# Optimization experiments

Measured on AMD Instinct MI355X. Metric: run time of the kernel, lower is better.

Reference implementation:

```python
import jax, jax.numpy as jnp
import numpy as np

EPS = 1e-5

def layernorm(x, w, b):
    mu = x.mean(-1, keepdims=True)
    var = x.var(-1, keepdims=True)
    return (x - mu) / jnp.sqrt(var + EPS) * w + b

def silu(x):
    return x * jax.nn.sigmoid(x)

def causal_dwconv(x, w, b):
    # x: (B,L,D), w: (D,K) depthwise causal conv along L
    K = w.shape[1]
    xt = jnp.moveaxis(x, 1, 2)                      # (B,D,L)
    xt = jnp.pad(xt, ((0, 0), (0, 0), (K - 1, 0)))
    y = jax.lax.conv_general_dilated(xt, w[:, None, :], (1,), 'VALID',
        dimension_numbers=('NCH', 'OIH', 'NCH'), feature_group_count=w.shape[0])
    return jnp.moveaxis(y + b[None, :, None], 2, 1)

def mamba_layer(x, p):
    # LayerNorm + Mamba selective scan; returns (out, C) with C the per-step C projection ("C_fast")
    xn = layernorm(x, p['ln_w'], p['ln_b'])
    xz = xn @ p['in_proj_w']                        # (B,L,2*Di)
    Di = p['conv_w'].shape[0]
    xh, z = xz[..., :Di], xz[..., Di:]
    xh = silu(causal_dwconv(xh, p['conv_w'], p['conv_b']))
    dbl = xh @ p['x_proj_w']                        # (B,L,R+2*S)
    R = p['dt_proj_w'].shape[0]
    S = p['A_log'].shape[1]
    dt = jax.nn.softplus(dbl[..., :R] @ p['dt_proj_w'] + p['dt_proj_b'])  # (B,L,Di)
    Bm = dbl[..., R:R + S]                          # (B,L,S)
    Cm = dbl[..., R + S:]                           # (B,L,S)
    A = -jnp.exp(p['A_log'])                        # (Di,S)
    dA = jnp.exp(dt[..., None] * A)                 # (B,L,Di,S)
    dBx = dt[..., None] * Bm[:, :, None, :] * xh[..., None]
    def step(h, inp):
        a, bx = inp
        h = a * h + bx
        return h, h
    h0 = jnp.zeros((x.shape[0], Di, S), x.dtype)
    _, hs = jax.lax.scan(step, h0, (jnp.moveaxis(dA, 1, 0), jnp.moveaxis(dBx, 1, 0)))
    y = jnp.einsum('lbds,bls->bld', hs, Cm) + p['D'] * xh
    y = y * silu(z)
    return y @ p['out_proj_w'], Cm

def run_chunks(x, k, p):
    # contiguous L-chunks folded into batch (chunks are independent sequences)
    B, L, D = x.shape
    y, C = mamba_layer(x.reshape(B * k, L // k, D), p)
    return y.reshape(B, L, D), C.reshape(B, k, L // k, -1)

def batchnorm(h, g, b):
    mu = h.mean((0, 1))
    var = h.var((0, 1))
    return (h - mu) / jnp.sqrt(var + EPS) * g + b

def freq_ffn(x, fc1_w, bn1_g, bn1_b, r_mat, i_mat, rb, ib, fc2_w, bn2_g, bn2_b):
    h = jax.nn.relu(batchnorm(jnp.einsum('bnc,hc->bnh', x, fc1_w), bn1_g, bn1_b))
    xf = jnp.fft.fft(h, axis=1, norm='ortho')
    # torch einsum 'bnc,cc->bnc' multiplies by the DIAGONAL of the matrix
    rd = jnp.diagonal(r_mat)
    idg = jnp.diagonal(i_mat)
    xr = jax.nn.relu(xf.real * rd - xf.imag * idg + rb)
    xi = jax.nn.relu(xf.imag * rd + xf.real * idg + ib)
    h = jnp.fft.ifft(xr + 1j * xi, axis=1, norm='ortho').real.astype(x.dtype)
    return batchnorm(jnp.einsum('bnh,ch->bnc', h, fc2_w), bn2_g, bn2_b)


def setup_inputs() -> dict:
    key = jax.random.key(0)
    B, L, D = 4, 512, 128
    Di, S, R, K, H = 256, 64, 8, 4, 256
    ks = jax.random.split(key, 16)
    rn = lambda k, sh, s=1.0: (jax.random.normal(k, sh) * s).astype(jnp.float32)
    return {
        'x': rn(ks[0], (B, L, D)),
        'ln_w': jnp.ones((D,), jnp.float32), 'ln_b': jnp.zeros((D,), jnp.float32),
        'in_proj_w': rn(ks[1], (D, 2 * Di), D ** -0.5),
        'conv_w': rn(ks[2], (Di, K), 0.3),
        'conv_b': jnp.zeros((Di,), jnp.float32),
        'x_proj_w': rn(ks[3], (Di, R + 2 * S), Di ** -0.5),
        'dt_proj_w': rn(ks[4], (R, Di), R ** -0.5),
        'dt_proj_b': rn(ks[5], (Di,), 0.1) - 4.0,
        'A_log': jnp.log(jnp.tile(jnp.arange(1, S + 1, dtype=jnp.float32), (Di, 1))),
        'D_param': jnp.ones((Di,), jnp.float32),
        'out_proj_w': rn(ks[6], (Di, D), Di ** -0.5),
        'norm1_w': jnp.ones((D,), jnp.float32), 'norm1_b': jnp.zeros((D,), jnp.float32),
        'norm2_w': jnp.ones((D,), jnp.float32), 'norm2_b': jnp.zeros((D,), jnp.float32),
        'fc1_w': rn(ks[7], (H, D), D ** -0.5),
        'bn1_g': jnp.ones((H,), jnp.float32), 'bn1_b': jnp.zeros((H,), jnp.float32),
        'r_mat': rn(ks[8], (H, H), 0.02),
        'i_mat': rn(ks[9], (H, H), 0.02),
        'rb': rn(ks[10], (H,), 0.02),
        'ib': rn(ks[11], (H,), 0.02),
        'fc2_w': rn(ks[12], (D, H), H ** -0.5),
        'bn2_g': jnp.ones((D,), jnp.float32), 'bn2_b': jnp.zeros((D,), jnp.float32),
    }


def reference(x, ln_w, ln_b, in_proj_w, conv_w, conv_b, x_proj_w, dt_proj_w, dt_proj_b,
              A_log, D_param, out_proj_w, norm1_w, norm1_b, norm2_w, norm2_b,
              fc1_w, bn1_g, bn1_b, r_mat, i_mat, rb, ib, fc2_w, bn2_g, bn2_b):
    p = dict(ln_w=ln_w, ln_b=ln_b, in_proj_w=in_proj_w, conv_w=conv_w, conv_b=conv_b,
             x_proj_w=x_proj_w, dt_proj_w=dt_proj_w, dt_proj_b=dt_proj_b,
             A_log=A_log, D=D_param, out_proj_w=out_proj_w)
    x_o, C0 = mamba_layer(x, p)                 # full sequence
    y1, C1 = run_chunks(x, 2, p)                # 2 halves
    y2, C2 = run_chunks(x, 4, p)                # 4 quarters
    y3, C3 = run_chunks(x, 8, p)                # 8 eighths
    x_o = x_o + y1 + y2 + y3                    # drop_path = Identity
    xo = x + layernorm(x_o, norm1_w, norm1_b)
    out = xo + freq_ffn(layernorm(xo, norm2_w, norm2_b),
                        fc1_w, bn1_g, bn1_b, r_mat, i_mat, rb, ib, fc2_w, bn2_g, bn2_b)
    return out, C0, C1, C2, C3
```

## Files before the change

kernel.cpp:

```cpp
#include <hip/hip_runtime.h>
#include <hip/hip_bf16.h>
#include <math.h>


constexpr int NT = 2048;
constexpr int Di = 256;
constexpr float EPSF = 1e-5f;
constexpr float LOG2E = 1.4426950408889634f;
constexpr float ISQ512 = 0.04419417382415922f;

typedef __attribute__((ext_vector_type(8))) short short8;
typedef __attribute__((ext_vector_type(4))) float f32x4;

constexpr long O_CS2B  = 0;
constexpr long O_CSIB  = 262144;
constexpr long O_A2    = 524288;
constexpr long O_FC1B  = 540672;
constexpr long O_FC2B  = 557056;
constexpr long O_INPB  = 573440;
constexpr long O_XPB2  = 606208;
constexpr long O_OPB   = 663552;
constexpr long O_RD    = 679936;
constexpr long O_IDG   = 680192;
constexpr long O_XNB   = 680448;
constexpr long O_XZB   = 811520;
constexpr long O_XHB   = 1335808;
constexpr long O_DBLX  = 2384384;
constexpr long O_DTDX  = 5595648;
constexpr long O_BCT   = 7692800;
constexpr long O_YS    = 8741376;
constexpr long O_XO    = 10838528;
constexpr long O_LN2B  = 11100672;
constexpr long O_H1B   = 11231744;
constexpr long O_H1NTB = 11493888;
constexpr long O_XRITB = 11756032;
constexpr long O_H2B   = 12280320;
constexpr long O_F2B   = 12542464;
constexpr long O_SQ1   = 12673536;
constexpr long O_SQ2   = 12674048;
constexpr long O_XO1   = O_XRITB;
constexpr long O_YACCB = O_DBLX;

__device__ __forceinline__ ushort bf16bits(float v) {
  __hip_bfloat16 h = __float2bfloat16(v);
  return *(ushort*)&h;
}
__device__ __forceinline__ float bfu(ushort u) {
  return __uint_as_float((uint)u << 16);
}

__global__ __launch_bounds__(256) void k_tables(
    const float* __restrict__ A_log, const float* __restrict__ fc1_w,
    const float* __restrict__ fc2_w, const float* __restrict__ r_mat,
    const float* __restrict__ i_mat, const float* __restrict__ in_proj_w,
    const float* __restrict__ x_proj_w, const float* __restrict__ dt_proj_w,
    const float* __restrict__ out_proj_w,
    const float* __restrict__ x, const float* __restrict__ ln_w,
    const float* __restrict__ ln_b, float* __restrict__ ws) {
  __shared__ float ct[512];
  int tid = threadIdx.x;
  ct[tid]       = __cosf((float)tid * (6.283185307179586f / 512.0f)) * ISQ512;
  ct[tid + 256] = __cosf((float)(tid + 256) * (6.283185307179586f / 512.0f)) * ISQ512;
  __syncthreads();
  __hip_bfloat16* cs2b = (__hip_bfloat16*)(ws + O_CS2B);
  __hip_bfloat16* csib = (__hip_bfloat16*)(ws + O_CSIB);
  int i = blockIdx.x * 256 + tid;
  if (i < 524288) {
    int r = i >> 9, n = i & 511;
    float v;
    if (r < 512) v = ct[(r * n) & 511];
    else         v = -ct[((r - 512) * n + 384) & 511];
    cs2b[i] = __float2bfloat16(v);
  } else {
    int j = i - 524288;
    int n = j >> 10, kp = j & 1023;
    float v;
    if (kp < 512) v = ct[(n * kp) & 511];
    else          v = -ct[(n * (kp - 512) + 384) & 511];
    csib[j] = __float2bfloat16(v);
  }
  if (i < 16384) ws[O_A2 + i] = -expf(A_log[i]) * LOG2E;
  if (i < 32768) {
    ((__hip_bfloat16*)(ws + O_FC1B))[i] = __float2bfloat16(fc1_w[i]);
    ((__hip_bfloat16*)(ws + O_FC2B))[i] = __float2bfloat16(fc2_w[i]);
  }
  if (i < 65536) {
    int n = i >> 7, k = i & 127;
    ((__hip_bfloat16*)(ws + O_INPB))[i] = __float2bfloat16(in_proj_w[k * 512 + n]);
  }
  if (i < 114688) {
    int n = i >> 8, k = i & 255;
    float v = 0.f;
    if (n < 136) v = x_proj_w[k * 136 + n];
    else if (n < 392) {
      int d = n - 136;
#pragma unroll
      for (int r = 0; r < 8; ++r) v = fmaf(x_proj_w[k * 136 + r], dt_proj_w[r * 256 + d], v);
    }
    ((__hip_bfloat16*)(ws + O_XPB2))[i] = __float2bfloat16(v);
  }
  if (i >= 131072 && i < 163840) {
    int j = i - 131072;
    int n = j >> 8, k = j & 255;
    ((__hip_bfloat16*)(ws + O_OPB))[j] = __float2bfloat16(out_proj_w[k * 128 + n]);
  }
  if (i < 256) {
    ws[O_RD + i] = r_mat[i * 256 + i];
    ws[O_IDG + i] = i_mat[i * 256 + i];
  }
  if (i < 512) ws[O_SQ1 + i] = 0.f;
  if (i < 256) ws[O_SQ2 + i] = 0.f;
  if (blockIdx.x < 512) {
    ushort* outb = (ushort*)(ws + O_XNB);
    int lane = tid & 63;
    int t = (blockIdx.x * 256 + tid) >> 6;
    float v0 = x[t * 128 + lane], v1 = x[t * 128 + 64 + lane];
    float s = v0 + v1, sq = v0 * v0 + v1 * v1;
#pragma unroll
    for (int off = 32; off; off >>= 1) { s += __shfl_xor(s, off); sq += __shfl_xor(sq, off); }
    float mu = s * (1.f / 128.f);
    float rstd = rsqrtf(sq * (1.f / 128.f) - mu * mu + EPSF);
    outb[t * 128 + lane]      = bf16bits((v0 - mu) * rstd * ln_w[lane] + ln_b[lane]);
    outb[t * 128 + 64 + lane] = bf16bits((v1 - mu) * rstd * ln_w[64 + lane] + ln_b[64 + lane]);
  }
}

__global__ void k_lndbl(const float* __restrict__ x, const float* __restrict__ xo1,
                        const float* __restrict__ w1, const float* __restrict__ b1,
                        const float* __restrict__ w2, const float* __restrict__ b2,
                        float* __restrict__ xo, ushort* __restrict__ ln2b) {
  int lane = threadIdx.x & 63;
  int t = (blockIdx.x * 256 + threadIdx.x) >> 6;
  float u0 = xo1[t * 128 + lane], u1 = xo1[t * 128 + 64 + lane];
  float s = u0 + u1, sq = u0 * u0 + u1 * u1;
#pragma unroll
  for (int off = 32; off; off >>= 1) { s += __shfl_xor(s, off); sq += __shfl_xor(sq, off); }
  float mu = s * (1.f / 128.f);
  float rstd = rsqrtf(sq * (1.f / 128.f) - mu * mu + EPSF);
  float a0 = x[t * 128 + lane]      + (u0 - mu) * rstd * w1[lane] + b1[lane];
  float a1 = x[t * 128 + 64 + lane] + (u1 - mu) * rstd * w1[64 + lane] + b1[64 + lane];
  xo[t * 128 + lane] = a0;
  xo[t * 128 + 64 + lane] = a1;
  s = a0 + a1; sq = a0 * a0 + a1 * a1;
#pragma unroll
  for (int off = 32; off; off >>= 1) { s += __shfl_xor(s, off); sq += __shfl_xor(sq, off); }
  mu = s * (1.f / 128.f);
  rstd = rsqrtf(sq * (1.f / 128.f) - mu * mu + EPSF);
  ln2b[t * 128 + lane]      = bf16bits((a0 - mu) * rstd * w2[lane] + b2[lane]);
  ln2b[t * 128 + 64 + lane] = bf16bits((a1 - mu) * rstd * w2[64 + lane] + b2[64 + lane]);
}

template <bool OUTBF16>
__global__ __launch_bounds__(256) void k_gmfma(const ushort* __restrict__ A,
                                               const ushort* __restrict__ Bt,
                                               void* __restrict__ Cv,
                                               int M, int N, int K,
                                               long sA, long sBt, long sC) {
  A += (long)blockIdx.z * sA;
  Bt += (long)blockIdx.z * sBt;
  int lane = threadIdx.x & 63, wid = threadIdx.x >> 6;
  int m0 = blockIdx.y * 64 + wid * 16, n0 = blockIdx.x * 64;
  const ushort* arow = A + (long)(m0 + (lane & 15)) * K + (lane >> 4) * 8;
  const ushort* brow = Bt + (long)(n0 + (lane & 15)) * K + (lane >> 4) * 8;
  f32x4 acc0 = {0.f, 0.f, 0.f, 0.f}, acc1 = acc0, acc2 = acc0, acc3 = acc0;
#pragma unroll 4
  for (int k0 = 0; k0 < K; k0 += 32) {
    short8 av = *(const short8*)(arow + k0);
    short8 b0 = *(const short8*)(brow + k0);
    short8 b1 = *(const short8*)(brow + 16L * K + k0);
    short8 b2 = *(const short8*)(brow + 32L * K + k0);
    short8 b3 = *(const short8*)(brow + 48L * K + k0);
    acc0 = __builtin_amdgcn_mfma_f32_16x16x32_bf16(av, b0, acc0, 0, 0, 0);
    acc1 = __builtin_amdgcn_mfma_f32_16x16x32_bf16(av, b1, acc1, 0, 0, 0);
    acc2 = __builtin_amdgcn_mfma_f32_16x16x32_bf16(av, b2, acc2, 0, 0, 0);
    acc3 = __builtin_amdgcn_mfma_f32_16x16x32_bf16(av, b3, acc3, 0, 0, 0);
  }
  int r0 = (lane >> 4) * 4, c0 = lane & 15;
#pragma unroll
  for (int j = 0; j < 4; ++j) {
    long row = m0 + r0 + j;
    float v[4] = {acc0[j], acc1[j], acc2[j], acc3[j]};
    if (OUTBF16) {
      __hip_bfloat16* C = (__hip_bfloat16*)Cv + blockIdx.z * sC;
#pragma unroll
      for (int c = 0; c < 4; ++c) {
        int n = n0 + c * 16 + c0;
        if (n < N) C[row * N + n] = __float2bfloat16(v[c]);
      }
    } else {
      float* C = (float*)Cv + blockIdx.z * sC;
#pragma unroll
      for (int c = 0; c < 4; ++c) {
        int n = n0 + c * 16 + c0;
        if (n < N) C[row * N + n] = v[c];
      }
    }
  }
}

__global__ __launch_bounds__(256) void k_gmfma_bn(const ushort* __restrict__ A,
                                                  const ushort* __restrict__ Bt,
                                                  ushort* __restrict__ C,
                                                  float* __restrict__ SQ,
                                                  int N, int K) {
  int lane = threadIdx.x & 63, wid = threadIdx.x >> 6;
  int m0 = blockIdx.y * 64 + wid * 16, n0 = blockIdx.x * 64;
  const ushort* arow = A + (long)(m0 + (lane & 15)) * K + (lane >> 4) * 8;
  const ushort* brow = Bt + (long)(n0 + (lane & 15)) * K + (lane >> 4) * 8;
  f32x4 acc[4] = {{0.f, 0.f, 0.f, 0.f}, {0.f, 0.f, 0.f, 0.f},
                  {0.f, 0.f, 0.f, 0.f}, {0.f, 0.f, 0.f, 0.f}};
#pragma unroll 4
  for (int k0 = 0; k0 < K; k0 += 32) {
    short8 av = *(const short8*)(arow + k0);
#pragma unroll
    for (int c = 0; c < 4; ++c) {
      short8 bv = *(const short8*)(brow + (long)c * 16 * K + k0);
      acc[c] = __builtin_amdgcn_mfma_f32_16x16x32_bf16(av, bv, acc[c], 0, 0, 0);
    }
  }
  int r0 = (lane >> 4) * 4, c0 = lane & 15;
#pragma unroll
  for (int j = 0; j < 4; ++j) {
    long row = m0 + r0 + j;
#pragma unroll
    for (int c = 0; c < 4; ++c)
      C[row * N + n0 + c * 16 + c0] = bf16bits(acc[c][j]);
  }
#pragma unroll
  for (int c = 0; c < 4; ++c) {
    f32x4 v = acc[c];
    float s = v[0] + v[1] + v[2] + v[3];
    float q = v[0] * v[0] + v[1] * v[1] + v[2] * v[2] + v[3] * v[3];
    s += __shfl_xor(s, 16); s += __shfl_xor(s, 32);
    q += __shfl_xor(q, 16); q += __shfl_xor(q, 32);
    if ((lane >> 4) == 0) {
      int n = n0 + c * 16 + c0;
      atomicAdd(&SQ[n], s);
      atomicAdd(&SQ[N + n], q);
    }
  }
}

__global__ void k_conv4(const ushort* __restrict__ xzb, const float* __restrict__ cw,
                        const float* __restrict__ cb, ushort* __restrict__ xhb) {
  int i = blockIdx.x * 256 + threadIdx.x;
  int t = i >> 8, d = i & 255;
  float w0 = cw[d * 4 + 0], w1 = cw[d * 4 + 1], w2 = cw[d * 4 + 2], w3 = cw[d * 4 + 3];
  float bias = cb[d];
  float x0  = bfu(xzb[(long)t * 512 + d]);
  float xm1 = t >= 1 ? bfu(xzb[(long)(t - 1) * 512 + d]) : 0.f;
  float xm2 = t >= 2 ? bfu(xzb[(long)(t - 2) * 512 + d]) : 0.f;
  float xm3 = t >= 3 ? bfu(xzb[(long)(t - 3) * 512 + d]) : 0.f;
  if ((t & 63) >= 3) {
    float s = fmaf(w0, xm3, fmaf(w1, xm2, fmaf(w2, xm1, fmaf(w3, x0, bias))));
    float sil = s / (1.f + expf(-s));
    ushort sb = bf16bits(sil);
#pragma unroll
    for (int v = 0; v < 4; ++v) xhb[v * 524288 + i] = sb;
  } else {
#pragma unroll
    for (int v = 0; v < 4; ++v) {
      int lv = t & ((512 >> v) - 1);
      float s = fmaf(w3, x0, bias);
      if (lv >= 1) s = fmaf(w2, xm1, s);
      if (lv >= 2) s = fmaf(w1, xm2, s);
      if (lv >= 3) s = fmaf(w0, xm3, s);
      float sil = s / (1.f + expf(-s));
      xhb[v * 524288 + i] = bf16bits(sil);
    }
  }
}

__global__ __launch_bounds__(256) void k_prep(const float* __restrict__ dblx,
                                              const ushort* __restrict__ xhb,
                                              const float* __restrict__ dt_b,
                                              float* __restrict__ outC,
                                              uint* __restrict__ DTDX,
                                              float* __restrict__ BCT) {
  int t0 = blockIdx.x * 64, task = blockIdx.y, v = blockIdx.z;
  int tid = threadIdx.x;
  const float* dp = dblx + ((long)v * 2048 + t0) * 392;
  if (task < 4) {
    __shared__ uint tile[64][65];
    int d0 = task * 64;
#pragma unroll
    for (int it = 0; it < 16; ++it) {
      int idx = it * 256 + tid;
      int t = idx >> 6, dl = idx & 63;
      int d = d0 + dl;
      float logit = dp[(long)t * 392 + 136 + d] + dt_b[d];
      float dtv = fmaxf(logit, 0.f) + log1pf(expf(-fabsf(logit)));
      float xv = bfu(xhb[((long)v * 2048 + t0 + t) * 256 + d]);
      tile[t][dl] = ((uint)bf16bits(dtv * xv) << 16) | (uint)bf16bits(dtv);
    }
    __syncthreads();
#pragma unroll
    for (int it = 0; it < 16; ++it) {
      int idx = it * 256 + tid;
      int dl = idx >> 6, t = idx & 63;
      DTDX[((long)(v * 256 + d0 + dl)) * 2048 + t0 + t] = tile[t][dl];
    }
  } else if (task < 6) {
    int j0 = (task - 4) * 64;
    float* bout = BCT + ((long)v * 2048 + t0) * 128;
#pragma unroll
    for (int it = 0; it < 16; ++it) {
      int idx = it * 256 + tid;
      int t = idx >> 6, j = (idx & 63) + j0;
      bout[(long)t * 128 + j] = dp[(long)t * 392 + 8 + j];
    }
  } else {
#pragma unroll
    for (int it = 0; it < 16; ++it) {
      int idx = it * 256 + tid;
      int t = idx >> 6, s = idx & 63;
      outC[(long)v * 131072 + (long)(t0 + t) * 64 + s] = dp[(long)t * 392 + 72 + s];
    }
  }
}

template <int CTRL>
__device__ __forceinline__ float dpp_add(float x) {
  int t = __builtin_amdgcn_update_dpp(0, __float_as_int(x), CTRL, 0xF, 0xF, true);
  return x + __int_as_float(t);
}

__global__ __launch_bounds__(256) void k_scan(const uint* __restrict__ DTDX,
                                              const float* __restrict__ BCT,
                                              const float* __restrict__ A2,
                                              float* __restrict__ ys) {
  int lane = threadIdx.x & 63;
  int gwid = (blockIdx.x * 256 + threadIdx.x) >> 6;
  int v, base;
  if (gwid < 1024)      { v = 0; base = 0; }
  else if (gwid < 3072) { v = 1; base = 1024; }
  else if (gwid < 7168) { v = 2; base = 3072; }
  else                  { v = 3; base = 7168; }
  int local = gwid - base;
  int b = local >> 8, d = local & 255;
  int Lp = 512 >> v;
  int t0 = b * Lp;
  const uint* drow = DTDX + ((long)(v * 256 + d)) * 2048 + t0;
  const float* brow = BCT + ((long)(v * 2048 + t0)) * 128;
  float* ysp = ys + (long)v * NT * Di + (long)((b << 8) + d) * Lp;
  float a2 = A2[d * 64 + lane];
  float h = 0.f;

#define LOADG(BB, CC, G)                                                     \
  { const float* rg = rowp + (G) * 1024;                                     \
    _Pragma("unroll") for (int q = 0; q < 8; ++q) {                          \
      BB[q] = rg[q * 128 + lane];                                            \
      CC[q] = rg[q * 128 + 64 + lane];                                       \
    } }
#define PROCG(BB, CC, G)                                                     \
  _Pragma("unroll") for (int q = 0; q < 8; ++q) {                            \
    const int l2 = (G) * 8 + q;                                              \
    uint u = (uint)__builtin_amdgcn_readlane((int)rdx, l2);                  \
    float sdt = __uint_as_float(u << 16);                                    \
    float sdx = __uint_as_float(u & 0xffff0000u);                            \
    float a = __builtin_amdgcn_exp2f(sdt * a2);                              \
    h = fmaf(a, h, sdx * BB[q]);                                             \
    float p = h * CC[q];                                                     \
    p = dpp_add<0x111>(p); p = dpp_add<0x112>(p);                            \
    p = dpp_add<0x114>(p); p = dpp_add<0x118>(p);                            \
    p = dpp_add<0x142>(p); p = dpp_add<0x143>(p);                            \
    int tot = __builtin_amdgcn_readlane(__float_as_int(p), 63);              \
    asm("v_writelane_b32 %0, %1, %2" : "+v"(ybuf_i) : "s"(tot), "i"(l2));    \
  }

  for (int c = 0; c < Lp; c += 64) {
    uint rdx = drow[c + lane];
    const float* rowp = brow + (long)c * 128;
    int ybuf_i = 0;
    float b0[8], c0[8], b1[8], c1[8];
    LOADG(b0, c0, 0)
    LOADG(b1, c1, 1)
    PROCG(b0, c0, 0) LOADG(b0, c0, 2)
    PROCG(b1, c1, 1) LOADG(b1, c1, 3)
    PROCG(b0, c0, 2) LOADG(b0, c0, 4)
    PROCG(b1, c1, 3) LOADG(b1, c1, 5)
    PROCG(b0, c0, 4) LOADG(b0, c0, 6)
    PROCG(b1, c1, 5) LOADG(b1, c1, 7)
    PROCG(b0, c0, 6)
    PROCG(b1, c1, 7)
    ysp[c + lane] = __int_as_float(ybuf_i);
  }
#undef LOADG
#undef PROCG
}

__global__ void k_yfull(const float* __restrict__ ys, const ushort* __restrict__ xhb,
                        const ushort* __restrict__ xzb, const float* __restrict__ Dp,
                        ushort* __restrict__ yaccb) {
  int i = blockIdx.x * 256 + threadIdx.x;
  int t = i >> 8, d = i & 255;
  float z = bfu(xzb[(long)t * 512 + 256 + d]);
  float sil = z / (1.f + expf(-z));
  float Dd = Dp[d];
  float s = 0.f;
#pragma unroll
  for (int v = 0; v < 4; ++v) {
    int Lp = 512 >> v;
    int b = t >> (9 - v);
    int l = t & (Lp - 1);
    float ysv = ys[(long)v * NT * Di + (long)((b << 8) + d) * Lp + l];
    float xhv = bfu(xhb[(long)v * 524288 + i]);
    s += ysv + Dd * xhv;
  }
  yaccb[i] = bf16bits(s * sil);
}

__global__ __launch_bounds__(256) void k_bnreluT(const ushort* __restrict__ h1b,
                                                 const float* __restrict__ SQ,
                                                 const float* __restrict__ g,
                                                 const float* __restrict__ bb,
                                                 ushort* __restrict__ outT) {
  __shared__ float tile[64][65];
  __shared__ float sc_s[64], sh_s[64];
  int t0 = blockIdx.x * 64, f0 = blockIdx.y * 64, b = blockIdx.z;
  int tid = threadIdx.x;
  if (tid < 64) {
    int f = f0 + tid;
    float mu = SQ[f] * (1.f / NT);
    float var = SQ[256 + f] * (1.f / NT) - mu * mu;
    float sc = g[f] * rsqrtf(var + EPSF);
    sc_s[tid] = sc;
    sh_s[tid] = bb[f] - mu * sc;
  }
  __syncthreads();
  const uint* h1u = (const uint*)h1b;
#pragma unroll
  for (int i = 0; i < 8; ++i) {
    int idx = i * 256 + tid;
    int r = idx >> 5, cu = idx & 31;
    uint u = h1u[((long)(b * 512 + t0 + r)) * 128 + (f0 >> 1) + cu];
    int c = cu * 2;
    tile[r][c]     = fmaxf(fmaf(bfu((ushort)(u & 0xffff)), sc_s[c], sh_s[c]), 0.f);
    tile[r][c + 1] = fmaxf(fmaf(bfu((ushort)(u >> 16)), sc_s[c + 1], sh_s[c + 1]), 0.f);
  }
  __syncthreads();
  int tc2 = (tid & 31) * 2, fr0 = tid >> 5;
#pragma unroll
  for (int i = 0; i < 8; ++i) {
    int fr = fr0 + i * 8;
    uint u = ((uint)bf16bits(tile[tc2 + 1][fr]) << 16) | bf16bits(tile[tc2][fr]);
    long off = (long)b * 131072 + (long)(f0 + fr) * 512 + t0 + tc2;
    *(uint*)(outT + off) = u;
  }
}

__global__ __launch_bounds__(256) void k_dftfreq(const ushort* __restrict__ CS2B,
                                                 const ushort* __restrict__ H1NTB,
                                                 const float* __restrict__ rd,
                                                 const float* __restrict__ idg,
                                                 const float* __restrict__ rb,
                                                 const float* __restrict__ ib,
                                                 ushort* __restrict__ XRITB) {
  int b = blockIdx.z;
  int lane = threadIdx.x & 63, wid = threadIdx.x >> 6;
  int m0 = blockIdx.y * 64 + wid * 16;
  int n0 = blockIdx.x * 64;
  const ushort* acrow = CS2B + (long)(m0 + (lane & 15)) * 512 + (lane >> 4) * 8;
  const ushort* asrow = acrow + 512L * 512;
  const ushort* brow = H1NTB + (long)b * 131072 + (long)(n0 + (lane & 15)) * 512 + (lane >> 4) * 8;
  f32x4 aC[4] = {{0.f, 0.f, 0.f, 0.f}, {0.f, 0.f, 0.f, 0.f},
                 {0.f, 0.f, 0.f, 0.f}, {0.f, 0.f, 0.f, 0.f}};
  f32x4 aS[4] = {{0.f, 0.f, 0.f, 0.f}, {0.f, 0.f, 0.f, 0.f},
                 {0.f, 0.f, 0.f, 0.f}, {0.f, 0.f, 0.f, 0.f}};
#pragma unroll 2
  for (int k0 = 0; k0 < 512; k0 += 32) {
    short8 avc = *(const short8*)(acrow + k0);
    short8 avs = *(const short8*)(asrow + k0);
#pragma unroll
    for (int c = 0; c < 4; ++c) {
      short8 bv = *(const short8*)(brow + (long)c * 16 * 512 + k0);
      aC[c] = __builtin_amdgcn_mfma_f32_16x16x32_bf16(avc, bv, aC[c], 0, 0, 0);
      aS[c] = __builtin_amdgcn_mfma_f32_16x16x32_bf16(avs, bv, aS[c], 0, 0, 0);
    }
  }
  int r0 = (lane >> 4) * 4, c0 = lane & 15;
#pragma unroll
  for (int c = 0; c < 4; ++c) {
    int f = n0 + c * 16 + c0;
    float rdv = rd[f], idv = idg[f], rbv = rb[f], ibv = ib[f];
    ushort pr[4], pi[4];
#pragma unroll
    for (int j = 0; j < 4; ++j) {
      float xr = aC[c][j], xi = aS[c][j];
      pr[j] = bf16bits(fmaxf(xr * rdv - xi * idv + rbv, 0.f));
      pi[j] = bf16bits(fmaxf(xi * rdv + xr * idv + ibv, 0.f));
    }
    long base = (long)b * 262144 + (long)f * 1024 + m0 + r0;
    uint2 ur = make_uint2(((uint)pr[1] << 16) | pr[0], ((uint)pr[3] << 16) | pr[2]);
    uint2 ui = make_uint2(((uint)pi[1] << 16) | pi[0], ((uint)pi[3] << 16) | pi[2]);
    *(uint2*)(XRITB + base) = ur;
    *(uint2*)(XRITB + base + 512) = ui;
  }
}

__global__ __launch_bounds__(256) void k_final(const float* __restrict__ xo,
                                               const ushort* __restrict__ f2b,
                                               const float* __restrict__ SQ,
                                               const float* __restrict__ g,
                                               const float* __restrict__ bb,
                                               float* __restrict__ out) {
  __shared__ float sc_s[128], sh_s[128];
  int tid = threadIdx.x;
  if (tid < 128) {
    float mu = SQ[tid] * (1.f / NT);
    float var = SQ[128 + tid] * (1.f / NT) - mu * mu;
    float sc = g[tid] * rsqrtf(var + EPSF);
    sc_s[tid] = sc;
    sh_s[tid] = bb[tid] - mu * sc;
  }
  __syncthreads();
  int i = blockIdx.x * 256 + tid;
  int c = i & 127;
  out[i] = xo[i] + fmaf(bfu(f2b[i]), sc_s[c], sh_s[c]);
}

extern "C" void kernel_launch(void* const* d_in, const int* in_sizes, int n_in,
                              void* d_out, int out_size, void* d_ws, size_t ws_size,
                              hipStream_t stream) {
  const float* x         = (const float*)d_in[0];
  const float* ln_w      = (const float*)d_in[1];
  const float* ln_b      = (const float*)d_in[2];
  const float* in_proj_w = (const float*)d_in[3];
  const float* conv_w    = (const float*)d_in[4];
  const float* conv_b    = (const float*)d_in[5];
  const float* x_proj_w  = (const float*)d_in[6];
  const float* dt_proj_w = (const float*)d_in[7];
  const float* dt_proj_b = (const float*)d_in[8];
  const float* A_log     = (const float*)d_in[9];
  const float* D_param   = (const float*)d_in[10];
  const float* out_proj_w= (const float*)d_in[11];
  const float* n1w       = (const float*)d_in[12];
  const float* n1b       = (const float*)d_in[13];
  const float* n2w       = (const float*)d_in[14];
  const float* n2b       = (const float*)d_in[15];
  const float* fc1_w     = (const float*)d_in[16];
  const float* bn1_g     = (const float*)d_in[17];
  const float* bn1_b     = (const float*)d_in[18];
  const float* r_mat     = (const float*)d_in[19];
  const float* i_mat     = (const float*)d_in[20];
  const float* rb        = (const float*)d_in[21];
  const float* ib        = (const float*)d_in[22];
  const float* fc2_w     = (const float*)d_in[23];
  const float* bn2_g     = (const float*)d_in[24];
  const float* bn2_b     = (const float*)d_in[25];
  float* ws  = (float*)d_ws;
  float* out = (float*)d_out;

  k_tables<<<4096, 256, 0, stream>>>(A_log, fc1_w, fc2_w, r_mat, i_mat,
                                     in_proj_w, x_proj_w, dt_proj_w, out_proj_w,
                                     x, ln_w, ln_b, ws);
  k_gmfma<true><<<dim3(8, 32, 1), 256, 0, stream>>>(
      (const ushort*)(ws + O_XNB), (const ushort*)(ws + O_INPB), ws + O_XZB,
      2048, 512, 128, 0, 0, 0);
  k_conv4<<<2048, 256, 0, stream>>>((const ushort*)(ws + O_XZB), conv_w, conv_b,
                                    (ushort*)(ws + O_XHB));
  k_gmfma<false><<<dim3(7, 32, 4), 256, 0, stream>>>(
      (const ushort*)(ws + O_XHB), (const ushort*)(ws + O_XPB2), ws + O_DBLX,
      2048, 392, 256, 524288L, 0, 802816L);
  k_prep<<<dim3(32, 7, 4), 256, 0, stream>>>(ws + O_DBLX, (const ushort*)(ws + O_XHB),
                                             dt_proj_b, out + 262144,
                                             (uint*)(ws + O_DTDX), ws + O_BCT);
  k_scan<<<3840, 256, 0, stream>>>((const uint*)(ws + O_DTDX), ws + O_BCT,
                                   ws + O_A2, ws + O_YS);
  k_yfull<<<2048, 256, 0, stream>>>(ws + O_YS, (const ushort*)(ws + O_XHB),
                                    (const ushort*)(ws + O_XZB), D_param,
                                    (ushort*)(ws + O_YACCB));
  k_gmfma<false><<<dim3(2, 32, 1), 256, 0, stream>>>(
      (const ushort*)(ws + O_YACCB), (const ushort*)(ws + O_OPB), ws + O_XO1,
      2048, 128, 256, 0, 0, 0);
  k_lndbl<<<512, 256, 0, stream>>>(x, ws + O_XO1, n1w, n1b, n2w, n2b,
                                   ws + O_XO, (ushort*)(ws + O_LN2B));
  k_gmfma_bn<<<dim3(4, 32), 256, 0, stream>>>(
      (const ushort*)(ws + O_LN2B), (const ushort*)(ws + O_FC1B),
      (ushort*)(ws + O_H1B), ws + O_SQ1, 256, 128);
  k_bnreluT<<<dim3(8, 4, 4), 256, 0, stream>>>((const ushort*)(ws + O_H1B),
                                               ws + O_SQ1, bn1_g, bn1_b,
                                               (ushort*)(ws + O_H1NTB));
  k_dftfreq<<<dim3(4, 8, 4), 256, 0, stream>>>(
      (const ushort*)(ws + O_CS2B), (const ushort*)(ws + O_H1NTB),
      ws + O_RD, ws + O_IDG, rb, ib, (ushort*)(ws + O_XRITB));
  k_gmfma<true><<<dim3(4, 8, 4), 256, 0, stream>>>(
      (const ushort*)(ws + O_CSIB), (const ushort*)(ws + O_XRITB), ws + O_H2B,
      512, 256, 1024, 0, 262144L, 131072L);
  k_gmfma_bn<<<dim3(2, 32), 256, 0, stream>>>(
      (const ushort*)(ws + O_H2B), (const ushort*)(ws + O_FC2B),
      (ushort*)(ws + O_F2B), ws + O_SQ2, 128, 256);
  k_final<<<1024, 256, 0, stream>>>(ws + O_XO, (const ushort*)(ws + O_F2B),
                                    ws + O_SQ2, bn2_g, bn2_b, out);
}
```

Baseline: 295.7 us.

## Unfold dt_proj from x_proj GEMM and compute rank-8 dt in prep kernel

The x_proj GEMM previously used a weight pre-multiplied by dt_proj, producing 392 output columns per token, and k_prep read the 256 dt logits back from memory. Now the GEMM produces only the 136 x_proj columns. k_prep recomputes the dt logits as an 8-term dot product from shared-memory copies of the rank-8 projection and the dt_proj weights. This cuts GEMM work and the write and read of the large intermediate buffer, at the cost of a few extra FMAs and an extra sync in k_prep. The BCT copy is also merged into a single task per block.

```diff
diff --git a/kernel.cpp b/kernel.cpp
--- a/kernel.cpp
+++ b/kernel.cpp
@@ -18,28 +18,28 @@
 constexpr long O_FC1B  = 540672;
 constexpr long O_FC2B  = 557056;
 constexpr long O_INPB  = 573440;
-constexpr long O_XPB2  = 606208;
-constexpr long O_OPB   = 663552;
-constexpr long O_RD    = 679936;
-constexpr long O_IDG   = 680192;
-constexpr long O_XNB   = 680448;
-constexpr long O_XZB   = 811520;
-constexpr long O_XHB   = 1335808;
-constexpr long O_DBLX  = 2384384;
-constexpr long O_DTDX  = 5595648;
-constexpr long O_BCT   = 7692800;
-constexpr long O_YS    = 8741376;
-constexpr long O_XO    = 10838528;
-constexpr long O_LN2B  = 11100672;
-constexpr long O_H1B   = 11231744;
-constexpr long O_H1NTB = 11493888;
-constexpr long O_XRITB = 11756032;
-constexpr long O_H2B   = 12280320;
-constexpr long O_F2B   = 12542464;
-constexpr long O_SQ1   = 12673536;
-constexpr long O_SQ2   = 12674048;
+constexpr long O_XPB   = 606208;
+constexpr long O_OPB   = 630784;
+constexpr long O_RD    = 647168;
+constexpr long O_IDG   = 647424;
+constexpr long O_XNB   = 647680;
+constexpr long O_XZB   = 778752;
+constexpr long O_XHB   = 1303040;
+constexpr long O_DBL   = 2351616;
+constexpr long O_DTDX  = 3465728;
+constexpr long O_BCT   = 5562880;
+constexpr long O_YS    = 6611456;
+constexpr long O_XO    = 8708608;
+constexpr long O_LN2B  = 8970752;
+constexpr long O_H1B   = 9101824;
+constexpr long O_H1NTB = 9363968;
+constexpr long O_XRITB = 9626112;
+constexpr long O_H2B   = 10150400;
+constexpr long O_F2B   = 10412544;
+constexpr long O_SQ1   = 10543616;
+constexpr long O_SQ2   = 10544128;
 constexpr long O_XO1   = O_XRITB;
-constexpr long O_YACCB = O_DBLX;
+constexpr long O_YACCB = O_DBL;
 
 __device__ __forceinline__ ushort bf16bits(float v) {
   __hip_bfloat16 h = __float2bfloat16(v);
@@ -53,8 +53,7 @@
     const float* __restrict__ A_log, const float* __restrict__ fc1_w,
     const float* __restrict__ fc2_w, const float* __restrict__ r_mat,
     const float* __restrict__ i_mat, const float* __restrict__ in_proj_w,
-    const float* __restrict__ x_proj_w, const float* __restrict__ dt_proj_w,
-    const float* __restrict__ out_proj_w,
+    const float* __restrict__ x_proj_w, const float* __restrict__ out_proj_w,
     const float* __restrict__ x, const float* __restrict__ ln_w,
     const float* __restrict__ ln_b, float* __restrict__ ws) {
   __shared__ float ct[512];
@@ -88,19 +87,13 @@
     int n = i >> 7, k = i & 127;
     ((__hip_bfloat16*)(ws + O_INPB))[i] = __float2bfloat16(in_proj_w[k * 512 + n]);
   }
-  if (i < 114688) {
+  if (i < 49152) {
     int n = i >> 8, k = i & 255;
-    float v = 0.f;
-    if (n < 136) v = x_proj_w[k * 136 + n];
-    else if (n < 392) {
-      int d = n - 136;
-#pragma unroll
-      for (int r = 0; r < 8; ++r) v = fmaf(x_proj_w[k * 136 + r], dt_proj_w[r * 256 + d], v);
-    }
-    ((__hip_bfloat16*)(ws + O_XPB2))[i] = __float2bfloat16(v);
-  }
-  if (i >= 131072 && i < 163840) {
-    int j = i - 131072;
+    float v = (n < 136) ? x_proj_w[k * 136 + n] : 0.f;
+    ((__hip_bfloat16*)(ws + O_XPB))[i] = __float2bfloat16(v);
+  }
+  if (i >= 65536 && i < 98304) {
+    int j = i - 65536;
     int n = j >> 8, k = j & 255;
     ((__hip_bfloat16*)(ws + O_OPB))[j] = __float2bfloat16(out_proj_w[k * 128 + n]);
   }
@@ -271,25 +264,42 @@
   }
 }
 
-__global__ __launch_bounds__(256) void k_prep(const float* __restrict__ dblx,
+__global__ __launch_bounds__(256) void k_prep(const float* __restrict__ dbl,
                                               const ushort* __restrict__ xhb,
+                                              const float* __restrict__ dtw,
                                               const float* __restrict__ dt_b,
                                               float* __restrict__ outC,
                                               uint* __restrict__ DTDX,
                                               float* __restrict__ BCT) {
   int t0 = blockIdx.x * 64, task = blockIdx.y, v = blockIdx.z;
   int tid = threadIdx.x;
-  const float* dp = dblx + ((long)v * 2048 + t0) * 392;
+  const float* dp = dbl + ((long)v * 2048 + t0) * 136;
   if (task < 4) {
+    __shared__ float r8T[8][64];
+    __shared__ float wt[8][64];
     __shared__ uint tile[64][65];
     int d0 = task * 64;
+    if (tid < 128) {
+      int t = tid >> 1, half = tid & 1;
+      float4 q = *(const float4*)&dp[(long)t * 136 + half * 4];
+      r8T[half * 4 + 0][t] = q.x; r8T[half * 4 + 1][t] = q.y;
+      r8T[half * 4 + 2][t] = q.z; r8T[half * 4 + 3][t] = q.w;
+    } else {
+      int idx = tid - 128;
+      int r = idx >> 4, dl4 = (idx & 15) * 4;
+      float4 q = *(const float4*)&dtw[r * 256 + d0 + dl4];
+      wt[r][dl4] = q.x; wt[r][dl4 + 1] = q.y; wt[r][dl4 + 2] = q.z; wt[r][dl4 + 3] = q.w;
+    }
+    __syncthreads();
 #pragma unroll
     for (int it = 0; it < 16; ++it) {
       int idx = it * 256 + tid;
       int t = idx >> 6, dl = idx & 63;
       int d = d0 + dl;
-      float logit = dp[(long)t * 392 + 136 + d] + dt_b[d];
-      float dtv = fmaxf(logit, 0.f) + log1pf(expf(-fabsf(logit)));
+      float s = dt_b[d];
+#pragma unroll
+      for (int r = 0; r < 8; ++r) s = fmaf(r8T[r][t], wt[r][dl], s);
+      float dtv = fmaxf(s, 0.f) + log1pf(expf(-fabsf(s)));
       float xv = bfu(xhb[((long)v * 2048 + t0 + t) * 256 + d]);
       tile[t][dl] = ((uint)bf16bits(dtv * xv) << 16) | (uint)bf16bits(dtv);
     }
@@ -300,21 +310,20 @@
       int dl = idx >> 6, t = idx & 63;
       DTDX[((long)(v * 256 + d0 + dl)) * 2048 + t0 + t] = tile[t][dl];
     }
-  } else if (task < 6) {
-    int j0 = (task - 4) * 64;
+  } else if (task == 4) {
     float* bout = BCT + ((long)v * 2048 + t0) * 128;
 #pragma unroll
-    for (int it = 0; it < 16; ++it) {
+    for (int it = 0; it < 32; ++it) {
       int idx = it * 256 + tid;
-      int t = idx >> 6, j = (idx & 63) + j0;
-      bout[(long)t * 128 + j] = dp[(long)t * 392 + 8 + j];
+      int t = idx >> 7, j = idx & 127;
+      bout[idx] = dp[(long)t * 136 + 8 + j];
     }
   } else {
 #pragma unroll
     for (int it = 0; it < 16; ++it) {
       int idx = it * 256 + tid;
       int t = idx >> 6, s = idx & 63;
-      outC[(long)v * 131072 + (long)(t0 + t) * 64 + s] = dp[(long)t * 392 + 72 + s];
+      outC[(long)v * 131072 + (long)(t0 + t) * 64 + s] = dp[(long)t * 136 + 72 + s];
     }
   }
 }
@@ -552,18 +561,18 @@
   float* out = (float*)d_out;
 
   k_tables<<<4096, 256, 0, stream>>>(A_log, fc1_w, fc2_w, r_mat, i_mat,
-                                     in_proj_w, x_proj_w, dt_proj_w, out_proj_w,
+                                     in_proj_w, x_proj_w, out_proj_w,
                                      x, ln_w, ln_b, ws);
   k_gmfma<true><<<dim3(8, 32, 1), 256, 0, stream>>>(
       (const ushort*)(ws + O_XNB), (const ushort*)(ws + O_INPB), ws + O_XZB,
       2048, 512, 128, 0, 0, 0);
   k_conv4<<<2048, 256, 0, stream>>>((const ushort*)(ws + O_XZB), conv_w, conv_b,
                                     (ushort*)(ws + O_XHB));
-  k_gmfma<false><<<dim3(7, 32, 4), 256, 0, stream>>>(
-      (const ushort*)(ws + O_XHB), (const ushort*)(ws + O_XPB2), ws + O_DBLX,
-      2048, 392, 256, 524288L, 0, 802816L);
-  k_prep<<<dim3(32, 7, 4), 256, 0, stream>>>(ws + O_DBLX, (const ushort*)(ws + O_XHB),
-                                             dt_proj_b, out + 262144,
+  k_gmfma<false><<<dim3(3, 32, 4), 256, 0, stream>>>(
+      (const ushort*)(ws + O_XHB), (const ushort*)(ws + O_XPB), ws + O_DBL,
+      2048, 136, 256, 524288L, 0, 278528L);
+  k_prep<<<dim3(32, 6, 4), 256, 0, stream>>>(ws + O_DBL, (const ushort*)(ws + O_XHB),
+                                             dt_proj_w, dt_proj_b, out + 262144,
                                              (uint*)(ws + O_DTDX), ws + O_BCT);
   k_scan<<<3840, 256, 0, stream>>>((const uint*)(ws + O_DTDX), ws + O_BCT,
                                    ws + O_A2, ws + O_YS);
```

After: 287.5 us. -2.8%, faster.
